# Optimization experiments

Hardware: AMD Instinct MI355X
Metric: run time of the kernel (lower is better)

The kernel has to match this reference:

```python
import jax, jax.numpy as jnp
import numpy as np

N = 65536      # nodes
M = 65536      # memory nodes (== N, so no padding branch)
D = 256        # dim_model
H = 8          # heads
DK = D // H    # 32
DFF = 1024
E1 = 1048576   # intra edges
E2 = 524288    # inter edges
MAX_ETYPE = 1000
EPS = 1e-5
SCALE = 1.0 / float(np.sqrt(DK))


def layer_norm(x, g, b):
    mu = jnp.mean(x, axis=-1, keepdims=True)
    var = jnp.mean((x - mu) ** 2, axis=-1, keepdims=True)
    return (x - mu) * jax.lax.rsqrt(var + EPS) * g + b


def graph_attention(q, k, v, src, dst, n_dst, e_rel=None):
    # q: [Nq,H,DK]; k,v: [Nk,H,DK]; src/dst: [E]
    e = jnp.einsum('ehd,ehd->eh', k[src], q[dst])  # masked_mm
    if e_rel is not None:
        e = e + e_rel                               # node_mul_edge bias
    e = e * SCALE
    # segment softmax over incoming edges per destination (sparse_softmax)
    m = jax.ops.segment_max(e, dst, num_segments=n_dst)
    ex = jnp.exp(e - m[dst])
    denom = jax.ops.segment_sum(ex, dst, num_segments=n_dst)
    a = ex / denom[dst]                             # [E,H]
    # vec_spmm: aggregate a * v[src] into dst
    return jax.ops.segment_sum(a[:, :, None] * v[src], dst, num_segments=n_dst)


def setup_inputs() -> dict:
    key = jax.random.key(0)
    ks = jax.random.split(key, 24)
    w = lambda k, shp, fan: jax.random.normal(k, shp, jnp.float32) * (1.0 / np.sqrt(fan))
    inp = {
        'h': jax.random.normal(ks[0], (N, D), jnp.float32),
        'mem': jax.random.normal(ks[1], (M, D), jnp.float32),
        'src_intra': jax.random.randint(ks[2], (E1,), 0, N, jnp.int32),
        'dst_intra': jax.random.randint(ks[3], (E1,), 0, N, jnp.int32),
        'etype': jax.random.randint(ks[4], (E1,), 0, MAX_ETYPE, jnp.int32),
        'src_inter': jax.random.randint(ks[5], (E2,), 0, M, jnp.int32),
        'dst_inter': jax.random.randint(ks[6], (E2,), 0, N, jnp.int32),
        # intra-attention projections (branch 0)
        'Wq0': w(ks[7], (D, D), D), 'Wk0': w(ks[8], (D, D), D),
        'Wv0': w(ks[9], (D, D), D), 'Wo0': w(ks[10], (D, D), D),
        # inter-attention projections (branch 1)
        'Wq1': w(ks[11], (D, D), D), 'Wk1': w(ks[12], (D, D), D),
        'Wv1': w(ks[13], (D, D), D), 'Wo1': w(ks[14], (D, D), D),
        'ak_embed': jax.random.normal(ks[15], (MAX_ETYPE, DK), jnp.float32) * 0.02,
        # layer norms: norm_in[0], norm_in[1], norm_inter
        'ln0_g': jnp.ones((D,), jnp.float32), 'ln0_b': jnp.zeros((D,), jnp.float32),
        'ln1_g': jnp.ones((D,), jnp.float32), 'ln1_b': jnp.zeros((D,), jnp.float32),
        'ln2_g': jnp.ones((D,), jnp.float32), 'ln2_b': jnp.zeros((D,), jnp.float32),
        # FFN
        'Wf1': w(ks[16], (D, DFF), D), 'bf1': jnp.zeros((DFF,), jnp.float32),
        'Wf2': w(ks[17], (DFF, D), DFF), 'bf2': jnp.zeros((D,), jnp.float32),
    }
    return inp


def reference(h, mem, Wq0, Wk0, Wv0, Wo0, Wq1, Wk1, Wv1, Wo1, ak_embed,
              ln0_g, ln0_b, ln1_g, ln1_b, ln2_g, ln2_b,
              Wf1, bf1, Wf2, bf2,
              src_intra, dst_intra, etype, src_inter, dst_inter):
    # ---- intra (self) graph attention ----
    q = (h @ Wq0).reshape(-1, H, DK)
    k = (h @ Wk0).reshape(-1, H, DK)
    v = (h @ Wv0).reshape(-1, H, DK)
    ak = ak_embed[etype]                                   # [E1, DK]
    e_rel = jnp.einsum('ed,ehd->eh', ak, q[dst_intra])     # rel-pos bias
    a = graph_attention(q, k, v, src_intra, dst_intra, N, e_rel)
    o = a.reshape(-1, D) @ Wo0
    h = layer_norm(h + o, ln0_g, ln0_b)
    # ---- inter (memory) graph attention ----  (M == N: no padding)
    q = (h @ Wq1).reshape(-1, H, DK)
    k = (mem @ Wk1).reshape(-1, H, DK)
    v = (mem @ Wv1).reshape(-1, H, DK)
    a = graph_attention(q, k, v, src_inter, dst_inter, N)
    o = a.reshape(-1, D) @ Wo1
    h = layer_norm(h + o, ln1_g, ln1_b)
    # ---- FFN + norm_inter ----
    ffn = jax.nn.relu(h @ Wf1 + bf1) @ Wf2 + bf2
    h = layer_norm(h + ffn, ln2_g, ln2_b)
    return h
```

## Files before the change

kernel.cpp:

```cpp
#include <hip/hip_runtime.h>

#define N_NODES 65536
#define D_MODEL 256
#define DFF     1024
#define E1_N    1048576
#define E2_N    524288
#define ATT_SCALE 0.17677669529663687f
#define LN_EPS  1e-5f

typedef __attribute__((ext_vector_type(8))) __bf16 bf16x8;
typedef __attribute__((ext_vector_type(4))) float  floatx4;
typedef __attribute__((ext_vector_type(4))) unsigned short ushortx4;
typedef __attribute__((ext_vector_type(8))) unsigned short ushortx8;

__device__ __forceinline__ float bf2f(unsigned short u) {
  return __uint_as_float(((unsigned)u) << 16);
}
__device__ __forceinline__ unsigned short f2bf(float f) {
  unsigned u = __float_as_uint(f);
  return (unsigned short)((u + 0x7FFFu + ((u >> 16) & 1u)) >> 16);
}
__device__ __forceinline__ int dot4i8(unsigned a, unsigned b, int c) {
#if __has_builtin(__builtin_amdgcn_sdot4)
  return __builtin_amdgcn_sdot4((int)a, (int)b, c, false);
#else
  c += (int)(signed char)(a & 0xFF) * (int)(signed char)(b & 0xFF);
  c += (int)(signed char)((a >> 8) & 0xFF) * (int)(signed char)((b >> 8) & 0xFF);
  c += (int)(signed char)((a >> 16) & 0xFF) * (int)(signed char)((b >> 16) & 0xFF);
  c += (int)(signed char)(a >> 24) * (int)(signed char)(b >> 24);
  return c;
#endif
}
__device__ __forceinline__ unsigned pack4i8(float a, float b, float c, float d, float inv) {
  int r0 = __float2int_rn(a * inv) & 0xFF;
  int r1 = __float2int_rn(b * inv) & 0xFF;
  int r2 = __float2int_rn(c * inv) & 0xFF;
  int r3 = __float2int_rn(d * inv) & 0xFF;
  return (unsigned)(r0 | (r1 << 8) | (r2 << 16) | (r3 << 24));
}

__device__ __forceinline__ void gld_lds16(const void* g, void* l) {
  __builtin_amdgcn_global_load_lds(
      (const __attribute__((address_space(1))) unsigned int*)g,
      (__attribute__((address_space(3))) unsigned int*)l, 16, 0, 0);
}

struct TW8 {
  const float* w[8];
  unsigned short* o[8];
};
__global__ __launch_bounds__(256) void transpose8(TW8 t) {
  __shared__ float tile[32][33];
  const int z = blockIdx.z;
  const float* W = t.w[z];
  unsigned short* Wt = t.o[z];
  const int tx = threadIdx.x & 31;
  const int ty = threadIdx.x >> 5;
  const int r0 = blockIdx.y * 32;
  const int c0 = blockIdx.x * 32;
#pragma unroll
  for (int p = 0; p < 4; ++p) {
    const int r = ty + p * 8;
    tile[r][tx] = W[(size_t)(r0 + r) * 256 + c0 + tx];
  }
  __syncthreads();
#pragma unroll
  for (int p = 0; p < 4; ++p) {
    const int r = ty + p * 8;
    Wt[(size_t)(c0 + r) * 256 + r0 + tx] = f2bf(tile[tx][r]);
  }
}

__global__ __launch_bounds__(256) void transpose_w(const float* __restrict__ W,
                                                   unsigned short* __restrict__ Wt,
                                                   int K, int Nc) {
  __shared__ float tile[32][33];
  const int tx = threadIdx.x & 31;
  const int ty = threadIdx.x >> 5;
  const int r0 = blockIdx.y * 32;
  const int c0 = blockIdx.x * 32;
#pragma unroll
  for (int p = 0; p < 4; ++p) {
    const int r = ty + p * 8;
    tile[r][tx] = W[(size_t)(r0 + r) * Nc + c0 + tx];
  }
  __syncthreads();
#pragma unroll
  for (int p = 0; p < 4; ++p) {
    const int r = ty + p * 8;
    Wt[(size_t)(c0 + r) * K + r0 + tx] = f2bf(tile[tx][r]);
  }
}

__global__ __launch_bounds__(256) void f2bf2_kernel(const float* __restrict__ in0,
                                                    unsigned short* __restrict__ out0,
                                                    const float* __restrict__ in1,
                                                    unsigned short* __restrict__ out1,
                                                    int half) {
  int i = blockIdx.x * 256 + threadIdx.x;
  const float* in = (i < half) ? in0 : in1;
  unsigned short* out = (i < half) ? out0 : out1;
  int k = (i < half) ? i : i - half;
  float4 v = ((const float4*)in)[k];
  ushortx4 o;
  o.x = f2bf(v.x); o.y = f2bf(v.y); o.z = f2bf(v.z); o.w = f2bf(v.w);
  ((ushortx4*)out)[k] = o;
}

__global__ __launch_bounds__(256) void zero_kernel(int* __restrict__ p, int n) {
  int i = blockIdx.x * 256 + threadIdx.x;
  if (i < n) p[i] = 0;
}

__global__ __launch_bounds__(256) void hist2_kernel(const int* __restrict__ d0,
                                                    int* __restrict__ c0,
                                                    const int* __restrict__ d1,
                                                    int* __restrict__ c1) {
  int e = blockIdx.x * 256 + threadIdx.x;
  if (e < E1_N) atomicAdd(&c0[d0[e]], 1);
  if (e < E2_N) atomicAdd(&c1[d1[e]], 1);
}

__global__ __launch_bounds__(1024) void scan2_kernel(int* __restrict__ cnt0,
                                                     int* __restrict__ rs0,
                                                     int* __restrict__ cur0,
                                                     int* __restrict__ cnt1,
                                                     int* __restrict__ rs1,
                                                     int* __restrict__ cur1) {
  int* cnt = blockIdx.x ? cnt1 : cnt0;
  int* row_start = blockIdx.x ? rs1 : rs0;
  int* cur = blockIdx.x ? cur1 : cur0;
  const int total = blockIdx.x ? E2_N : E1_N;
  __shared__ int lds[1024];
  const int tid = threadIdx.x;
  const int base = tid * 64;
  int s = 0;
  for (int i = 0; i < 64; ++i) s += cnt[base + i];
  lds[tid] = s;
  __syncthreads();
  int v = s;
  for (int off = 1; off < 1024; off <<= 1) {
    int add = (tid >= off) ? lds[tid - off] : 0;
    __syncthreads();
    v += add;
    lds[tid] = v;
    __syncthreads();
  }
  int run = v - s;
  for (int i = 0; i < 64; ++i) {
    int c = cnt[base + i];
    row_start[base + i] = run;
    cur[base + i] = run;
    run += c;
  }
  if (tid == 1023) row_start[N_NODES] = total;
}

__global__ __launch_bounds__(256) void scatter2_kernel(const int* __restrict__ s0,
                                                       const int* __restrict__ d0,
                                                       const int* __restrict__ et,
                                                       int* __restrict__ cur0,
                                                       int2* __restrict__ out0,
                                                       const int* __restrict__ s1,
                                                       const int* __restrict__ d1,
                                                       int* __restrict__ cur1,
                                                       int* __restrict__ out1) {
  int e = blockIdx.x * 256 + threadIdx.x;
  if (e < E1_N) {
    int p = atomicAdd(&cur0[d0[e]], 1);
    out0[p] = make_int2(s0[e], et[e]);
  }
  if (e < E2_N) {
    int p = atomicAdd(&cur1[d1[e]], 1);
    out1[p] = s1[e];
  }
}

template <bool BIAS, bool RELU, bool OUT_KVQ>
__global__ __launch_bounds__(256) void gemm_bf16(const unsigned short* __restrict__ A,
                                                 const unsigned short* __restrict__ Bt,
                                                 const float* __restrict__ bias,
                                                 void* __restrict__ C,
                                                 float* __restrict__ sbuf,
                                                 int K, int Ntot) {
  __shared__ __align__(16) unsigned short sA[128 * 32];
  __shared__ __align__(16) unsigned short sB[128 * 32];
  const int tid  = threadIdx.x;
  const int wave = tid >> 6;
  const int lane = tid & 63;
  const int m0 = blockIdx.y * 128;
  const int n0 = blockIdx.x * 128;

  floatx4 acc[4][4] = {};

  const int l4r = lane >> 2;
  const int l4c = (lane & 3) * 8;
  const int fr = lane & 15;
  const int fk = (lane >> 4) * 8;
  const int wy = (wave >> 1) * 64;
  const int wx = (wave & 1) * 64;

  for (int k0 = 0; k0 < K; k0 += 32) {
#pragma unroll
    for (int c = 0; c < 2; ++c) {
      const int row = wave * 32 + c * 16;
      gld_lds16(A  + ((size_t)(m0 + row + l4r) * K + k0 + l4c), &sA[row * 32]);
      gld_lds16(Bt + ((size_t)(n0 + row + l4r) * K + k0 + l4c), &sB[row * 32]);
    }
    __syncthreads();
    bf16x8 af[4], bfv[4];
#pragma unroll
    for (int i = 0; i < 4; ++i) af[i]  = *(const bf16x8*)&sA[(wy + i * 16 + fr) * 32 + fk];
#pragma unroll
    for (int j = 0; j < 4; ++j) bfv[j] = *(const bf16x8*)&sB[(wx + j * 16 + fr) * 32 + fk];
#pragma unroll
    for (int i = 0; i < 4; ++i)
#pragma unroll
      for (int j = 0; j < 4; ++j)
        acc[i][j] = __builtin_amdgcn_mfma_f32_16x16x32_bf16(af[i], bfv[j], acc[i][j], 0, 0, 0);
    __syncthreads();
  }

  const int coln = lane & 15;
  const int rowq = (lane >> 4) * 4;

  if (OUT_KVQ) {
    unsigned char* Cb = (unsigned char*)C;
#pragma unroll
    for (int i = 0; i < 4; ++i) {
#pragma unroll
      for (int jp = 0; jp < 2; ++jp) {
        const int head = ((n0 + wx) >> 5) + jp;
        const int pidx = (head < 8) ? head * 2 : (head - 8) * 2 + 1;
#pragma unroll
        for (int r = 0; r < 4; ++r) {
          float am = fmaxf(fabsf(acc[i][2 * jp][r]), fabsf(acc[i][2 * jp + 1][r]));
          am = fmaxf(am, __shfl_xor(am, 1));
          am = fmaxf(am, __shfl_xor(am, 2));
          am = fmaxf(am, __shfl_xor(am, 4));
          am = fmaxf(am, __shfl_xor(am, 8));
          const int m = m0 + wy + i * 16 + rowq + r;
          const float inv = am > 0.f ? 127.f / am : 0.f;
#pragma unroll
          for (int jj = 0; jj < 2; ++jj) {
            const int j = 2 * jp + jj;
            const int n = n0 + wx + j * 16 + coln;
            const int qv = __float2int_rn(acc[i][j][r] * inv);
            Cb[(size_t)m * 512 + n] = (unsigned char)(signed char)qv;
          }
          if (coln == 0) {
            sbuf[(size_t)m * 16 + pidx] = am * (1.f / 127.f);
          }
        }
      }
    }
  } else {
    unsigned short* Cs = (unsigned short*)C;
#pragma unroll
    for (int j = 0; j < 4; ++j) {
      const int n = n0 + wx + j * 16 + coln;
      float bval = 0.f;
      if (BIAS) bval = bias[n];
#pragma unroll
      for (int i = 0; i < 4; ++i) {
        const int mbase = m0 + wy + i * 16 + rowq;
#pragma unroll
        for (int r = 0; r < 4; ++r) {
          float v = acc[i][j][r] + bval;
          if (RELU) v = fmaxf(v, 0.f);
          Cs[(size_t)(mbase + r) * Ntot + n] = f2bf(v);
        }
      }
    }
  }
}

template <bool HAS_REL>
__global__ __launch_bounds__(256) void attn_kernel(const unsigned short* qb,
                                                   const unsigned char* __restrict__ kvb,
                                                   const float* __restrict__ sbuf,
                                                   const int* __restrict__ row_start,
                                                   const int2* __restrict__ s_se,
                                                   const int* __restrict__ s_src,
                                                   const float* __restrict__ ak_embed,
                                                   unsigned short* outp) {
  const int lane = threadIdx.x & 63;
  const int wave = threadIdx.x >> 6;
  const int dst  = blockIdx.x * 4 + wave;
  const int eg   = lane >> 4;
  const int l    = lane & 15;
  const int doff = l * 16;

  const unsigned short* qrow = qb + (size_t)dst * 256 + doff;
  ushortx8 qu0 = *(const ushortx8*)qrow;
  ushortx8 qu1 = *(const ushortx8*)(qrow + 8);
  float q[16];
#pragma unroll
  for (int d = 0; d < 8; ++d) {
    q[d]     = bf2f(qu0[d]) * ATT_SCALE;
    q[d + 8] = bf2f(qu1[d]) * ATT_SCALE;
  }
  float qam = 0.f;
#pragma unroll
  for (int d = 0; d < 16; ++d) qam = fmaxf(qam, fabsf(q[d]));
  qam = fmaxf(qam, __shfl_xor(qam, 1));
  const float qs   = qam * (1.f / 127.f);
  const float qinv = qam > 0.f ? 127.f / qam : 0.f;
  unsigned qi[4];
#pragma unroll
  for (int c = 0; c < 4; ++c)
    qi[c] = pack4i8(q[4 * c], q[4 * c + 1], q[4 * c + 2], q[4 * c + 3], qinv);

  float a[16];
#pragma unroll
  for (int d = 0; d < 16; ++d) a[d] = 0.f;
  float lsum = 0.f;

  const int beg = row_start[dst], end = row_start[dst + 1];
  for (int j = beg; j < end; j += 4) {
    const int e = j + eg;
    const bool valid = e < end;
    const int ecl = valid ? e : (end - 1);
    int src, et = 0;
    if (HAS_REL) {
      int2 se = s_se[ecl];
      src = se.x; et = se.y;
    } else {
      src = s_src[ecl];
    }
    const unsigned char* kvrow = kvb + (size_t)src * 512;
    float2 sc = *(const float2*)(sbuf + (size_t)src * 16 + (l >> 1) * 2);
    uint4 ku = *(const uint4*)(kvrow + doff);
    uint4 vu = *(const uint4*)(kvrow + 256 + doff);
    int idot = 0;
    idot = dot4i8(ku.x, qi[0], idot);
    idot = dot4i8(ku.y, qi[1], idot);
    idot = dot4i8(ku.z, qi[2], idot);
    idot = dot4i8(ku.w, qi[3], idot);
    float part = (float)idot * (sc.x * qs);
    if (HAS_REL) {
      const float* ak = ak_embed + (size_t)et * 32 + (l & 1) * 16;
      float4 a0 = *(const float4*)ak;
      float4 a1 = *(const float4*)(ak + 4);
      float4 a2 = *(const float4*)(ak + 8);
      float4 a3 = *(const float4*)(ak + 12);
      part += a0.x * q[0]  + a0.y * q[1]  + a0.z * q[2]  + a0.w * q[3]
            + a1.x * q[4]  + a1.y * q[5]  + a1.z * q[6]  + a1.w * q[7]
            + a2.x * q[8]  + a2.y * q[9]  + a2.z * q[10] + a2.w * q[11]
            + a3.x * q[12] + a3.y * q[13] + a3.z * q[14] + a3.w * q[15];
    }
    part += __shfl_xor(part, 1);
    const float pw = valid ? __expf(part) : 0.f;
    lsum += pw;
    const float pwv = pw * sc.y;
    {
      unsigned u = vu.x;
      a[0] += pwv * (float)(signed char)(u & 0xFF);
      a[1] += pwv * (float)(signed char)((u >> 8) & 0xFF);
      a[2] += pwv * (float)(signed char)((u >> 16) & 0xFF);
      a[3] += pwv * (float)(signed char)(u >> 24);
      u = vu.y;
      a[4] += pwv * (float)(signed char)(u & 0xFF);
      a[5] += pwv * (float)(signed char)((u >> 8) & 0xFF);
      a[6] += pwv * (float)(signed char)((u >> 16) & 0xFF);
      a[7] += pwv * (float)(signed char)(u >> 24);
      u = vu.z;
      a[8]  += pwv * (float)(signed char)(u & 0xFF);
      a[9]  += pwv * (float)(signed char)((u >> 8) & 0xFF);
      a[10] += pwv * (float)(signed char)((u >> 16) & 0xFF);
      a[11] += pwv * (float)(signed char)(u >> 24);
      u = vu.w;
      a[12] += pwv * (float)(signed char)(u & 0xFF);
      a[13] += pwv * (float)(signed char)((u >> 8) & 0xFF);
      a[14] += pwv * (float)(signed char)((u >> 16) & 0xFF);
      a[15] += pwv * (float)(signed char)(u >> 24);
    }
  }
  lsum += __shfl_xor(lsum, 16);
  lsum += __shfl_xor(lsum, 32);
#pragma unroll
  for (int d = 0; d < 16; ++d) {
    a[d] += __shfl_xor(a[d], 16);
    a[d] += __shfl_xor(a[d], 32);
  }
  const float inv = lsum > 0.f ? 1.f / lsum : 0.f;
  if (eg == 0) {
    ushortx8 o0, o1;
#pragma unroll
    for (int d = 0; d < 8; ++d) {
      o0[d] = f2bf(a[d] * inv);
      o1[d] = f2bf(a[d + 8] * inv);
    }
    unsigned short* orow = outp + (size_t)dst * 256 + doff;
    *(ushortx8*)orow = o0;
    *(ushortx8*)(orow + 8) = o1;
  }
}

template <bool WRITE_BF>
__global__ __launch_bounds__(256) void ln_kernel(const float* __restrict__ xin,
                                                 const unsigned short* __restrict__ oin,
                                                 const float* __restrict__ g,
                                                 const float* __restrict__ b,
                                                 float* __restrict__ xout,
                                                 unsigned short* __restrict__ bfout) {
  const int lane = threadIdx.x & 63;
  const int wave = threadIdx.x >> 6;
  const size_t row  = (size_t)blockIdx.x * 4 + wave;
  const size_t base = row * 256 + lane * 4;
  float4 xv = *(const float4*)(xin + base);
  ushortx4 ou = *(const ushortx4*)(oin + base);
  const float x0 = xv.x + bf2f(ou.x), x1 = xv.y + bf2f(ou.y),
              x2 = xv.z + bf2f(ou.z), x3 = xv.w + bf2f(ou.w);
  float sum = x0 + x1 + x2 + x3;
  float ss  = x0 * x0 + x1 * x1 + x2 * x2 + x3 * x3;
#pragma unroll
  for (int m = 1; m <= 32; m <<= 1) {
    sum += __shfl_xor(sum, m);
    ss  += __shfl_xor(ss, m);
  }
  const float mu  = sum * (1.f / 256.f);
  const float var = ss * (1.f / 256.f) - mu * mu;
  const float rs  = rsqrtf(var + LN_EPS);
  float4 gv = *(const float4*)(g + lane * 4);
  float4 bv = *(const float4*)(b + lane * 4);
  const float y0 = (x0 - mu) * rs * gv.x + bv.x;
  const float y1 = (x1 - mu) * rs * gv.y + bv.y;
  const float y2 = (x2 - mu) * rs * gv.z + bv.z;
  const float y3 = (x3 - mu) * rs * gv.w + bv.w;
  *(float4*)(xout + base) = make_float4(y0, y1, y2, y3);
  if (WRITE_BF) {
    ushortx4 yo;
    yo.x = f2bf(y0); yo.y = f2bf(y1); yo.z = f2bf(y2); yo.w = f2bf(y3);
    *(ushortx4*)(bfout + base) = yo;
  }
}

extern "C" void kernel_launch(void* const* d_in, const int* in_sizes, int n_in,
                              void* d_out, int out_size, void* d_ws, size_t ws_size,
                              hipStream_t stream) {
  const float* h_in      = (const float*)d_in[0];
  const float* mem_in    = (const float*)d_in[1];
  const int*   src_intra = (const int*)d_in[2];
  const int*   dst_intra = (const int*)d_in[3];
  const int*   etype     = (const int*)d_in[4];
  const int*   src_inter = (const int*)d_in[5];
  const int*   dst_inter = (const int*)d_in[6];
  const float* Wq0 = (const float*)d_in[7];
  const float* Wk0 = (const float*)d_in[8];
  const float* Wv0 = (const float*)d_in[9];
  const float* Wo0 = (const float*)d_in[10];
  const float* Wq1 = (const float*)d_in[11];
  const float* Wk1 = (const float*)d_in[12];
  const float* Wv1 = (const float*)d_in[13];
  const float* Wo1 = (const float*)d_in[14];
  const float* akE = (const float*)d_in[15];
  const float* ln0_g = (const float*)d_in[16];
  const float* ln0_b = (const float*)d_in[17];
  const float* ln1_g = (const float*)d_in[18];
  const float* ln1_b = (const float*)d_in[19];
  const float* ln2_g = (const float*)d_in[20];
  const float* ln2_b = (const float*)d_in[21];
  const float* Wf1 = (const float*)d_in[22];
  const float* bf1 = (const float*)d_in[23];
  const float* Wf2 = (const float*)d_in[24];
  const float* bf2 = (const float*)d_in[25];

  char* p = (char*)d_ws;
  auto alloc = [&](size_t bytes) {
    char* r = p;
    p += (bytes + 255) & ~(size_t)255;
    return r;
  };

  unsigned short* wqkv0t = (unsigned short*)alloc((size_t)768 * 256 * 2);
  unsigned short* wo0t   = (unsigned short*)alloc((size_t)256 * 256 * 2);
  unsigned short* wq1t   = (unsigned short*)alloc((size_t)256 * 256 * 2);
  unsigned short* wkv1t  = (unsigned short*)alloc((size_t)512 * 256 * 2);
  unsigned short* wo1t   = (unsigned short*)alloc((size_t)256 * 256 * 2);
  unsigned short* wf1t   = (unsigned short*)alloc((size_t)1024 * 256 * 2);
  unsigned short* wf2t   = (unsigned short*)alloc((size_t)256 * 1024 * 2);

  int* cnt01 = (int*)alloc((size_t)2 * N_NODES * 4);
  int* cnt0 = cnt01;
  int* cnt1 = cnt01 + N_NODES;
  int* rs0   = (int*)alloc((size_t)(N_NODES + 1) * 4);
  int* cur0  = (int*)alloc((size_t)N_NODES * 4);
  int* rs1   = (int*)alloc((size_t)(N_NODES + 1) * 4);
  int* cur1  = (int*)alloc((size_t)N_NODES * 4);
  int2* sse0 = (int2*)alloc((size_t)E1_N * 8);
  int* ssrc1 = (int*)alloc((size_t)E2_N * 4);

  char* regionA = alloc((size_t)128 * 1024 * 1024);
  unsigned short* qbuf    = (unsigned short*)regionA;
  unsigned char*  kv0q    = (unsigned char*)(regionA + (size_t)33554432);
  unsigned char*  kv1q    = (unsigned char*)(regionA + (size_t)67108864);
  unsigned short* scratch = (unsigned short*)(regionA + (size_t)100663296);
  unsigned short* hidden  = (unsigned short*)regionA;
  float* sbuf0 = (float*)alloc((size_t)N_NODES * 16 * 4);
  float* sbuf1 = (float*)alloc((size_t)N_NODES * 16 * 4);
  unsigned short* buf2 = (unsigned short*)alloc((size_t)N_NODES * 256 * 2);
  unsigned short* buf3 = (unsigned short*)alloc((size_t)N_NODES * 256 * 2);

  float* hcur = (float*)d_out;

  const int TB = 256;

  TW8 tw;
  tw.w[0] = Wq0; tw.o[0] = wqkv0t;
  tw.w[1] = Wk0; tw.o[1] = wqkv0t + 65536;
  tw.w[2] = Wv0; tw.o[2] = wqkv0t + 131072;
  tw.w[3] = Wo0; tw.o[3] = wo0t;
  tw.w[4] = Wq1; tw.o[4] = wq1t;
  tw.w[5] = Wk1; tw.o[5] = wkv1t;
  tw.w[6] = Wv1; tw.o[6] = wkv1t + 65536;
  tw.w[7] = Wo1; tw.o[7] = wo1t;
  transpose8<<<dim3(8, 8, 8), TB, 0, stream>>>(tw);
  transpose_w<<<dim3(32, 8), TB, 0, stream>>>(Wf1, wf1t, 256, 1024);
  transpose_w<<<dim3(8, 32), TB, 0, stream>>>(Wf2, wf2t, 1024, 256);

  f2bf2_kernel<<<32768, TB, 0, stream>>>(h_in, buf2, mem_in, buf3, N_NODES * 256 / 4);

  zero_kernel<<<512, TB, 0, stream>>>(cnt01, 2 * N_NODES);
  hist2_kernel<<<E1_N / 256, TB, 0, stream>>>(dst_intra, cnt0, dst_inter, cnt1);
  scan2_kernel<<<2, 1024, 0, stream>>>(cnt0, rs0, cur0, cnt1, rs1, cur1);
  scatter2_kernel<<<E1_N / 256, TB, 0, stream>>>(src_intra, dst_intra, etype, cur0, sse0,
                                                 src_inter, dst_inter, cur1, ssrc1);

  gemm_bf16<false, false, false><<<dim3(2, 512), TB, 0, stream>>>(buf2, wqkv0t, nullptr, qbuf, nullptr, 256, 256);
  gemm_bf16<false, false, true><<<dim3(4, 512), TB, 0, stream>>>(buf2, wqkv0t + 65536, nullptr, kv0q, sbuf0, 256, 512);
  attn_kernel<true><<<16384, TB, 0, stream>>>(qbuf, kv0q, sbuf0, rs0, sse0, nullptr, akE, qbuf);
  gemm_bf16<false, false, false><<<dim3(2, 512), TB, 0, stream>>>(qbuf, wo0t, nullptr, scratch, nullptr, 256, 256);
  ln_kernel<true><<<16384, TB, 0, stream>>>(h_in, scratch, ln0_g, ln0_b, hcur, buf2);

  gemm_bf16<false, false, false><<<dim3(2, 512), TB, 0, stream>>>(buf2, wq1t, nullptr, qbuf, nullptr, 256, 256);
  gemm_bf16<false, false, true><<<dim3(4, 512), TB, 0, stream>>>(buf3, wkv1t, nullptr, kv1q, sbuf1, 256, 512);
  attn_kernel<false><<<16384, TB, 0, stream>>>(qbuf, kv1q, sbuf1, rs1, nullptr, ssrc1, nullptr, qbuf);
  gemm_bf16<false, false, false><<<dim3(2, 512), TB, 0, stream>>>(qbuf, wo1t, nullptr, scratch, nullptr, 256, 256);
  ln_kernel<true><<<16384, TB, 0, stream>>>(hcur, scratch, ln1_g, ln1_b, hcur, buf3);

  gemm_bf16<true, true, false><<<dim3(8, 512), TB, 0, stream>>>(buf3, wf1t, bf1, hidden, nullptr, 256, 1024);
  gemm_bf16<true, false, false><<<dim3(2, 512), TB, 0, stream>>>(hidden, wf2t, bf2, buf2, nullptr, 1024, 256);
  ln_kernel<false><<<16384, TB, 0, stream>>>(hcur, buf2, ln2_g, ln2_b, hcur, nullptr);
}
```

Before: 1.030 ms.

## Build CSR via two-level bucket sort with LDS-local counting

Replaces the global-atomic histogram/scan/scatter CSR construction with a two-pass bucketed sort. Edges are first binned into 128 coarse destination buckets using LDS histograms and per-block global offsets. Each bucket is then counted, scanned and scattered in shared memory to produce row starts and sorted edge lists. This is meant to replace millions of contended global atomics and random global scatters with mostly LDS atomics and localized writes, at the cost of an extra pass over a temporary binned buffer and packing dst/etype into 16-bit fields.

```diff
diff --git a/kernel.cpp b/kernel.cpp
--- a/kernel.cpp
+++ b/kernel.cpp
@@ -7,6 +7,10 @@
 #define E2_N    524288
 #define ATT_SCALE 0.17677669529663687f
 #define LN_EPS  1e-5f
+
+#define NBUCK   128
+#define BSHIFT  9
+#define DPB     512
 
 typedef __attribute__((ext_vector_type(8))) __bf16 bf16x8;
 typedef __attribute__((ext_vector_type(4))) float  floatx4;
@@ -112,67 +116,168 @@
   if (i < n) p[i] = 0;
 }
 
-__global__ __launch_bounds__(256) void hist2_kernel(const int* __restrict__ d0,
-                                                    int* __restrict__ c0,
-                                                    const int* __restrict__ d1,
-                                                    int* __restrict__ c1) {
-  int e = blockIdx.x * 256 + threadIdx.x;
-  if (e < E1_N) atomicAdd(&c0[d0[e]], 1);
-  if (e < E2_N) atomicAdd(&c1[d1[e]], 1);
-}
-
-__global__ __launch_bounds__(1024) void scan2_kernel(int* __restrict__ cnt0,
-                                                     int* __restrict__ rs0,
-                                                     int* __restrict__ cur0,
-                                                     int* __restrict__ cnt1,
-                                                     int* __restrict__ rs1,
-                                                     int* __restrict__ cur1) {
-  int* cnt = blockIdx.x ? cnt1 : cnt0;
-  int* row_start = blockIdx.x ? rs1 : rs0;
-  int* cur = blockIdx.x ? cur1 : cur0;
-  const int total = blockIdx.x ? E2_N : E1_N;
-  __shared__ int lds[1024];
+
+__global__ __launch_bounds__(256) void bucket_hist_kernel(const int* __restrict__ d0,
+                                                          int* __restrict__ bh0,
+                                                          const int* __restrict__ d1,
+                                                          int* __restrict__ bh1) {
+  __shared__ int h0[NBUCK], h1[NBUCK];
   const int tid = threadIdx.x;
-  const int base = tid * 64;
-  int s = 0;
-  for (int i = 0; i < 64; ++i) s += cnt[base + i];
-  lds[tid] = s;
-  __syncthreads();
-  int v = s;
-  for (int off = 1; off < 1024; off <<= 1) {
-    int add = (tid >= off) ? lds[tid - off] : 0;
+  if (tid < NBUCK) { h0[tid] = 0; h1[tid] = 0; }
+  __syncthreads();
+  const int base = blockIdx.x * 2048;
+#pragma unroll
+  for (int i = 0; i < 8; ++i) {
+    const int e = base + i * 256 + tid;
+    atomicAdd(&h0[d0[e] >> BSHIFT], 1);
+    if (e < E2_N) atomicAdd(&h1[d1[e] >> BSHIFT], 1);
+  }
+  __syncthreads();
+  if (tid < NBUCK) {
+    if (h0[tid]) atomicAdd(&bh0[tid], h0[tid]);
+  } else if (tid < 2 * NBUCK) {
+    const int t = tid - NBUCK;
+    if (h1[t]) atomicAdd(&bh1[t], h1[t]);
+  }
+}
+
+__global__ __launch_bounds__(256) void bucket_scan_kernel(const int* __restrict__ bh0,
+                                                          int* __restrict__ bs0,
+                                                          int* __restrict__ bc0,
+                                                          int* __restrict__ rs0,
+                                                          const int* __restrict__ bh1,
+                                                          int* __restrict__ bs1,
+                                                          int* __restrict__ bc1,
+                                                          int* __restrict__ rs1) {
+  __shared__ int l[2][NBUCK];
+  const int tid = threadIdx.x;
+  const int g = tid >> 7;
+  const int t = tid & 127;
+  const int* bh = g ? bh1 : bh0;
+  int* bs = g ? bs1 : bs0;
+  int* bc = g ? bc1 : bc0;
+  const int orig = bh[t];
+  int v = orig;
+  l[g][t] = v;
+  __syncthreads();
+  for (int off = 1; off < NBUCK; off <<= 1) {
+    const int add = (t >= off) ? l[g][t - off] : 0;
     __syncthreads();
     v += add;
-    lds[tid] = v;
+    l[g][t] = v;
     __syncthreads();
   }
-  int run = v - s;
-  for (int i = 0; i < 64; ++i) {
-    int c = cnt[base + i];
-    row_start[base + i] = run;
-    cur[base + i] = run;
-    run += c;
-  }
-  if (tid == 1023) row_start[N_NODES] = total;
-}
-
-__global__ __launch_bounds__(256) void scatter2_kernel(const int* __restrict__ s0,
-                                                       const int* __restrict__ d0,
-                                                       const int* __restrict__ et,
-                                                       int* __restrict__ cur0,
-                                                       int2* __restrict__ out0,
-                                                       const int* __restrict__ s1,
-                                                       const int* __restrict__ d1,
-                                                       int* __restrict__ cur1,
-                                                       int* __restrict__ out1) {
-  int e = blockIdx.x * 256 + threadIdx.x;
-  if (e < E1_N) {
-    int p = atomicAdd(&cur0[d0[e]], 1);
-    out0[p] = make_int2(s0[e], et[e]);
-  }
-  if (e < E2_N) {
-    int p = atomicAdd(&cur1[d1[e]], 1);
-    out1[p] = s1[e];
+  bs[t + 1] = v;
+  bc[t] = v - orig;
+  if (t == 0) bs[0] = 0;
+  if (tid == 0) rs0[N_NODES] = E1_N;
+  if (tid == 1) rs1[N_NODES] = E2_N;
+}
+
+template <bool INTRA>
+__global__ __launch_bounds__(256) void bin_kernel(const int* __restrict__ src,
+                                                  const int* __restrict__ dst,
+                                                  const int* __restrict__ et,
+                                                  int* __restrict__ bcur,
+                                                  void* __restrict__ outv) {
+  __shared__ int cnt[NBUCK], gbase[NBUCK], lcur[NBUCK];
+  const int tid = threadIdx.x;
+  const int base = blockIdx.x * 2048;
+  if (tid < NBUCK) { cnt[tid] = 0; lcur[tid] = 0; }
+  int d[8], bk[8];
+#pragma unroll
+  for (int i = 0; i < 8; ++i) d[i] = dst[base + i * 256 + tid];
+  __syncthreads();
+#pragma unroll
+  for (int i = 0; i < 8; ++i) {
+    bk[i] = d[i] >> BSHIFT;
+    atomicAdd(&cnt[bk[i]], 1);
+  }
+  __syncthreads();
+  if (tid < NBUCK) gbase[tid] = atomicAdd(&bcur[tid], cnt[tid]);
+  __syncthreads();
+  if (INTRA) {
+    int2* out = (int2*)outv;
+#pragma unroll
+    for (int i = 0; i < 8; ++i) {
+      const int e = base + i * 256 + tid;
+      const int loc = atomicAdd(&lcur[bk[i]], 1);
+      out[gbase[bk[i]] + loc] = make_int2(src[e], (d[i] & (DPB - 1)) | (et[e] << 16));
+    }
+  } else {
+    int* out = (int*)outv;
+#pragma unroll
+    for (int i = 0; i < 8; ++i) {
+      const int e = base + i * 256 + tid;
+      const int loc = atomicAdd(&lcur[bk[i]], 1);
+      out[gbase[bk[i]] + loc] = src[e] | ((d[i] & (DPB - 1)) << 16);
+    }
+  }
+}
+
+__global__ __launch_bounds__(256) void csr_build_kernel(const int2* __restrict__ binned0,
+                                                        const int* __restrict__ bs0,
+                                                        int* __restrict__ rs0,
+                                                        int2* __restrict__ out0,
+                                                        const int* __restrict__ binned1,
+                                                        const int* __restrict__ bs1,
+                                                        int* __restrict__ rs1,
+                                                        int* __restrict__ out1) {
+  __shared__ int cnt[DPB];
+  __shared__ int cur[DPB];
+  __shared__ int wsum[4];
+  const int tid = threadIdx.x;
+  const int g = blockIdx.x >> 7;
+  const int b = blockIdx.x & 127;
+  const int bb = g ? bs1[b] : bs0[b];
+  const int be = g ? bs1[b + 1] : bs0[b + 1];
+  cnt[tid] = 0;
+  cnt[tid + 256] = 0;
+  __syncthreads();
+  if (g == 0) {
+    for (int j = bb + tid; j < be; j += 256) {
+      atomicAdd(&cnt[binned0[j].y & (DPB - 1)], 1);
+    }
+  } else {
+    for (int j = bb + tid; j < be; j += 256) {
+      atomicAdd(&cnt[binned1[j] >> 16], 1);
+    }
+  }
+  __syncthreads();
+  const int lane = tid & 63;
+  const int wv = tid >> 6;
+  const int c0 = cnt[2 * tid];
+  const int c1 = cnt[2 * tid + 1];
+  const int s = c0 + c1;
+  int incl = s;
+#pragma unroll
+  for (int m = 1; m < 64; m <<= 1) {
+    const int u = __shfl_up(incl, m);
+    if (lane >= m) incl += u;
+  }
+  if (lane == 63) wsum[wv] = incl;
+  __syncthreads();
+  int wb = 0;
+  for (int w = 0; w < wv; ++w) wb += wsum[w];
+  const int e0 = bb + wb + (incl - s);
+  int* rs = g ? rs1 : rs0;
+  rs[(b << BSHIFT) + 2 * tid] = e0;
+  rs[(b << BSHIFT) + 2 * tid + 1] = e0 + c0;
+  cur[2 * tid] = e0;
+  cur[2 * tid + 1] = e0 + c0;
+  __syncthreads();
+  if (g == 0) {
+    for (int j = bb + tid; j < be; j += 256) {
+      const int2 w = binned0[j];
+      const int p = atomicAdd(&cur[w.y & (DPB - 1)], 1);
+      out0[p] = make_int2(w.x, w.y >> 16);
+    }
+  } else {
+    for (int j = bb + tid; j < be; j += 256) {
+      const int w = binned1[j];
+      const int p = atomicAdd(&cur[w >> 16], 1);
+      out1[p] = w & 0xFFFF;
+    }
   }
 }
 
@@ -481,17 +586,21 @@
   unsigned short* wf1t   = (unsigned short*)alloc((size_t)1024 * 256 * 2);
   unsigned short* wf2t   = (unsigned short*)alloc((size_t)256 * 1024 * 2);
 
-  int* cnt01 = (int*)alloc((size_t)2 * N_NODES * 4);
-  int* cnt0 = cnt01;
-  int* cnt1 = cnt01 + N_NODES;
   int* rs0   = (int*)alloc((size_t)(N_NODES + 1) * 4);
-  int* cur0  = (int*)alloc((size_t)N_NODES * 4);
   int* rs1   = (int*)alloc((size_t)(N_NODES + 1) * 4);
-  int* cur1  = (int*)alloc((size_t)N_NODES * 4);
   int2* sse0 = (int2*)alloc((size_t)E1_N * 8);
   int* ssrc1 = (int*)alloc((size_t)E2_N * 4);
+  int* bh01 = (int*)alloc((size_t)2 * NBUCK * 4);
+  int* bh0 = bh01;
+  int* bh1 = bh01 + NBUCK;
+  int* bs0 = (int*)alloc((size_t)(NBUCK + 1) * 4);
+  int* bs1 = (int*)alloc((size_t)(NBUCK + 1) * 4);
+  int* bc0 = (int*)alloc((size_t)NBUCK * 4);
+  int* bc1 = (int*)alloc((size_t)NBUCK * 4);
 
   char* regionA = alloc((size_t)128 * 1024 * 1024);
+  int2* binned0 = (int2*)regionA;
+  int*  binned1 = (int*)(regionA + (size_t)E1_N * 8);
   unsigned short* qbuf    = (unsigned short*)regionA;
   unsigned char*  kv0q    = (unsigned char*)(regionA + (size_t)33554432);
   unsigned char*  kv1q    = (unsigned char*)(regionA + (size_t)67108864);
@@ -521,11 +630,13 @@
 
   f2bf2_kernel<<<32768, TB, 0, stream>>>(h_in, buf2, mem_in, buf3, N_NODES * 256 / 4);
 
-  zero_kernel<<<512, TB, 0, stream>>>(cnt01, 2 * N_NODES);
-  hist2_kernel<<<E1_N / 256, TB, 0, stream>>>(dst_intra, cnt0, dst_inter, cnt1);
-  scan2_kernel<<<2, 1024, 0, stream>>>(cnt0, rs0, cur0, cnt1, rs1, cur1);
-  scatter2_kernel<<<E1_N / 256, TB, 0, stream>>>(src_intra, dst_intra, etype, cur0, sse0,
-                                                 src_inter, dst_inter, cur1, ssrc1);
+  zero_kernel<<<1, TB, 0, stream>>>(bh01, 2 * NBUCK);
+  bucket_hist_kernel<<<E1_N / 2048, TB, 0, stream>>>(dst_intra, bh0, dst_inter, bh1);
+  bucket_scan_kernel<<<1, TB, 0, stream>>>(bh0, bs0, bc0, rs0, bh1, bs1, bc1, rs1);
+  bin_kernel<true><<<E1_N / 2048, TB, 0, stream>>>(src_intra, dst_intra, etype, bc0, binned0);
+  bin_kernel<false><<<E2_N / 2048, TB, 0, stream>>>(src_inter, dst_inter, nullptr, bc1, binned1);
+  csr_build_kernel<<<2 * NBUCK, TB, 0, stream>>>(binned0, bs0, rs0, sse0,
+                                                 binned1, bs1, rs1, ssrc1);
 
   gemm_bf16<false, false, false><<<dim3(2, 512), TB, 0, stream>>>(buf2, wqkv0t, nullptr, qbuf, nullptr, 256, 256);
   gemm_bf16<false, false, true><<<dim3(4, 512), TB, 0, stream>>>(buf2, wqkv0t + 65536, nullptr, kv0q, sbuf0, 256, 512);
```

New measurement: 881.1 us. -14.4%, faster.
